# Optimization experiments

Measured on AMD Instinct MI355X. Metric: run time of the kernel, lower is better.

Reference implementation:

```python
import jax, jax.numpy as jnp
import numpy as np
from jax.scipy.special import logsumexp

NUM_STATES = 16
NUM_CHAINS = 8
NUM_NODES = 1500
NUM_ITERS = 500


def setup_inputs() -> dict:
    key = jax.random.key(0)
    k1, k2, k3, k4 = jax.random.split(key, 4)
    return {
        "unnormalized_state_init": jax.random.normal(k1, (NUM_STATES, NUM_CHAINS), jnp.float32),
        "unnormalized_chain_weights": jax.random.normal(k2, (NUM_ITERS, NUM_CHAINS), jnp.float32),
        "unnormalized_emission_matrix": jax.random.normal(k3, (NUM_STATES, 1, NUM_NODES), jnp.float32),
        "unnormalized_transition_matrix": jax.random.normal(k4, (NUM_CHAINS, NUM_STATES, NUM_STATES), jnp.float32),
    }


def reference(unnormalized_state_init, unnormalized_chain_weights,
              unnormalized_emission_matrix, unnormalized_transition_matrix):
    # log_transform_params: normalize each distribution in log domain
    log_state_init = jax.nn.log_softmax(unnormalized_state_init, axis=0)          # (S,C): over states
    log_chain_weights = jax.nn.log_softmax(unnormalized_chain_weights, axis=-1)   # (T,C): over chains
    log_emission = jax.nn.log_softmax(unnormalized_emission_matrix, axis=-1)      # (S,1,N): over nodes
    log_T_ = jax.nn.log_softmax(unnormalized_transition_matrix, axis=-1)          # (C,S,S): over next state

    T = unnormalized_chain_weights.shape[0]

    # chain-marginalized transition matrix (computed as in torch forward_model; not used downstream)
    log_mean_cw = logsumexp(log_chain_weights, axis=0) - jnp.log(jnp.asarray(T, log_chain_weights.dtype))
    _log_transition_matrix = logsumexp(log_T_ + log_mean_cw[:, None, None], axis=0)

    # sequential HMM prior recursion over tiny (S,C) state via scan
    def step(h, _):
        # h: (S,C) -> h.T: (C,S); logsumexp over previous-state axis
        new = logsumexp(h.T[:, :, None] + log_T_, axis=1).T  # (S,C)
        return new, new

    h0 = log_state_init
    _, hs = jax.lax.scan(step, h0, None, length=T - 1)
    log_hidden_state_probs = jnp.concatenate([h0[None], hs], axis=0)  # (T,S,C)

    # emission broadcast: (S,1,N) + (T,S,C,1) -> (T,S,C,N), then add chain weights
    log_observed_state_probs_ = (log_emission[None]
                                 + log_hidden_state_probs[..., None]
                                 + log_chain_weights[:, None, :, None])
    # marginalize over states then chains
    log_observed_state_probs = logsumexp(log_observed_state_probs_, axis=(1, 2))  # (T,N)
    return (log_observed_state_probs, log_observed_state_probs_, log_hidden_state_probs)
```

## Files before the change

### kernel.cpp

```cpp
#include <hip/hip_runtime.h>
#include <hip/hip_bf16.h>

#define S 16
#define C 8
#define SC 128
#define TT 500
#define NN 1500
#define CHUNK 25
#define NCHUNK 20

__device__ __forceinline__ float fexp2(float x) { return exp2f(x); }
__device__ __forceinline__ float flog2(float x) { return log2f(x); }

#define L2E 1.4426950408889634f
#define LN2 0.6931471805599453f

__global__ __launch_bounds__(256) void emission_kernel(
    const float* __restrict__ uem, float* __restrict__ lem)
{
    const int s0 = blockIdx.x;
    const float* row = uem + s0 * NN;
    const int tid = threadIdx.x;
    __shared__ float sm[4];
    __shared__ float ss[4];

    float m = -1e30f;
    for (int n = tid; n < NN; n += 256) m = fmaxf(m, row[n]);
#pragma unroll
    for (int off = 32; off >= 1; off >>= 1) m = fmaxf(m, __shfl_xor(m, off));
    if ((tid & 63) == 0) sm[tid >> 6] = m;
    __syncthreads();
    const float M = fmaxf(fmaxf(sm[0], sm[1]), fmaxf(sm[2], sm[3]));

    float acc = 0.f;
    for (int n = tid; n < NN; n += 256) acc += fexp2((row[n] - M) * L2E);
#pragma unroll
    for (int off = 32; off >= 1; off >>= 1) acc += __shfl_xor(acc, off);
    if ((tid & 63) == 0) ss[tid >> 6] = acc;
    __syncthreads();
    const float lse = M + flog2(ss[0] + ss[1] + ss[2] + ss[3]) * LN2;

    for (int n = tid; n < NN; n += 256) lem[s0 * NN + n] = row[n] - lse;
}

#define MM(dst, Asrc, Bsrc) do {                                          \
    __syncthreads();                                                      \
    {   const int c_ = tid >> 5; const int e0_ = tid & 31;                \
        for (int r_ = 0; r_ < 8; ++r_) {                                  \
            const int e_ = e0_ + (r_ << 5);                               \
            const int i_ = e_ >> 4; const int l_ = e_ & 15;               \
            float acc_ = 0.f;                                             \
            _Pragma("unroll")                                             \
            for (int s_ = 0; s_ < S; ++s_)                                \
                acc_ += Asrc[(c_ * S + i_) * S + s_] *                    \
                        Bsrc[(c_ * S + s_) * S + l_];                     \
            dst[(c_ * S + i_) * S + l_] = acc_;                          \
        } }                                                               \
} while (0)

__global__ __launch_bounds__(256) void hmm_setup(
    const float* __restrict__ usi,
    const float* __restrict__ ucw,
    const float* __restrict__ utm,
    float* __restrict__ ws_lcw,
    float* __restrict__ ws_pT,
    float* __restrict__ ws_q)
{
    __shared__ float bufT[C * S * S];
    __shared__ float bufX[C * S * S];
    __shared__ float bufY[C * S * S];
    __shared__ float bufZ[C * S * S];
    __shared__ float qbuf[C * S];
    const int tid = threadIdx.x;

    for (int t = tid; t < TT; t += 256) {
        float x[C]; float m = -1e30f;
#pragma unroll
        for (int cc = 0; cc < C; ++cc) { x[cc] = ucw[t * C + cc]; m = fmaxf(m, x[cc]); }
        float acc = 0.f;
#pragma unroll
        for (int cc = 0; cc < C; ++cc) acc += fexp2((x[cc] - m) * L2E);
        const float lse = m + flog2(acc) * LN2;
#pragma unroll
        for (int cc = 0; cc < C; ++cc) ws_lcw[t * C + cc] = x[cc] - lse;
    }

    if (tid < SC) {
        float x[S]; float m = -1e30f;
#pragma unroll
        for (int k = 0; k < S; ++k) { x[k] = utm[tid * S + k]; m = fmaxf(m, x[k]); }
        float acc = 0.f; float e[S];
#pragma unroll
        for (int k = 0; k < S; ++k) { e[k] = fexp2((x[k] - m) * L2E); acc += e[k]; }
        const float inv = 1.f / acc;
#pragma unroll
        for (int k = 0; k < S; ++k) {
            const float v = e[k] * inv;
            bufT[tid * S + k] = v;
            ws_pT[tid * S + k] = v;
        }
    }

    if (tid < C) {
        const int cc = tid;
        float x[S]; float m = -1e30f;
#pragma unroll
        for (int s0 = 0; s0 < S; ++s0) { x[s0] = usi[s0 * C + cc]; m = fmaxf(m, x[s0]); }
        float acc = 0.f; float e[S];
#pragma unroll
        for (int s0 = 0; s0 < S; ++s0) { e[s0] = fexp2((x[s0] - m) * L2E); acc += e[s0]; }
        const float inv = 1.f / acc;
#pragma unroll
        for (int s0 = 0; s0 < S; ++s0) {
            const float v = e[s0] * inv;
            qbuf[cc * S + s0] = v;
            ws_q[cc * S + s0] = v;
        }
    }

    MM(bufX, bufT, bufT);
    MM(bufY, bufX, bufX);
    MM(bufZ, bufY, bufY);
    MM(bufX, bufZ, bufZ);
    MM(bufY, bufX, bufZ);
    MM(bufX, bufY, bufT);
    __syncthreads();

    const int c5 = tid >> 4;
    const int l5 = tid & 15;
    float Acol[S];
    if (tid < 128) {
#pragma unroll
        for (int s0 = 0; s0 < S; ++s0) Acol[s0] = bufX[(c5 * S + s0) * S + l5];
    }
    for (int k = 1; k < NCHUNK; ++k) {
        float acc = 0.f;
        if (tid < 128) {
#pragma unroll
            for (int s0 = 0; s0 < S; ++s0) acc += qbuf[c5 * S + s0] * Acol[s0];
        }
        __syncthreads();
        if (tid < 128) {
            qbuf[c5 * S + l5] = acc;
            ws_q[k * SC + c5 * S + l5] = acc;
        }
        __syncthreads();
    }
}

__global__ __launch_bounds__(64) void hmm_chunks(
    const float* __restrict__ ws_pT,
    const float* __restrict__ ws_q,
    float* __restrict__ out3)
{
    const int k = blockIdx.x;
    const int lane = threadIdx.x;
    const int c = lane >> 3;
    const int j = lane & 7;

    float Ta[S], Tb[S];
#pragma unroll
    for (int s0 = 0; s0 < S; ++s0) {
        Ta[s0] = ws_pT[(c * S + s0) * S + j];
        Tb[s0] = ws_pT[(c * S + s0) * S + j + 8];
    }
    float pa = ws_q[k * SC + c * S + j];
    float pb = ws_q[k * SC + c * S + j + 8];

    const int base = c << 3;
    for (int i = 0; i < CHUNK; ++i) {
        float* o = out3 + (size_t)(k * CHUNK + i) * SC;
        o[j * C + c]       = flog2(pa) * LN2;
        o[(j + 8) * C + c] = flog2(pb) * LN2;
        if (i == CHUNK - 1) break;

        float pv[S];
#pragma unroll
        for (int q = 0; q < 8; ++q) {
            pv[q]     = __shfl(pa, base + q);
            pv[q + 8] = __shfl(pb, base + q);
        }
        float a0 = 0.f, a1 = 0.f, a2 = 0.f, a3 = 0.f;
        float b0 = 0.f, b1 = 0.f, b2 = 0.f, b3 = 0.f;
#pragma unroll
        for (int s0 = 0; s0 < S; s0 += 4) {
            a0 = fmaf(pv[s0],     Ta[s0],     a0);
            a1 = fmaf(pv[s0 + 1], Ta[s0 + 1], a1);
            a2 = fmaf(pv[s0 + 2], Ta[s0 + 2], a2);
            a3 = fmaf(pv[s0 + 3], Ta[s0 + 3], a3);
            b0 = fmaf(pv[s0],     Tb[s0],     b0);
            b1 = fmaf(pv[s0 + 1], Tb[s0 + 1], b1);
            b2 = fmaf(pv[s0 + 2], Tb[s0 + 2], b2);
            b3 = fmaf(pv[s0 + 3], Tb[s0 + 3], b3);
        }
        pa = (a0 + a1) + (a2 + a3);
        pb = (b0 + b1) + (b2 + b3);
    }
}

__global__ __launch_bounds__(128) void broadcast_kernel(
    const float* __restrict__ lem,
    const float* __restrict__ lcw,
    const float* __restrict__ h3,
    float* __restrict__ out1,
    float* __restrict__ out2)
{
    const int t = blockIdx.y;
    const int tid = threadIdx.x;
    __shared__ float hc[SC];
    __shared__ float Ws[S];
    if (tid < SC) hc[tid] = h3[t * SC + tid] + lcw[t * C + (tid & 7)];
    __syncthreads();
    if (tid < S) {
        float m = -1e30f;
#pragma unroll
        for (int cc = 0; cc < C; ++cc) m = fmaxf(m, hc[tid * C + cc]);
        float acc = 0.f;
#pragma unroll
        for (int cc = 0; cc < C; ++cc) acc += fexp2((hc[tid * C + cc] - m) * L2E);
        Ws[tid] = m + flog2(acc) * LN2;
    }
    __syncthreads();

    const int n4 = blockIdx.x * 128 + tid;
    if (n4 >= 375) return;

    float4 es[S];
#pragma unroll
    for (int s0 = 0; s0 < S; ++s0)
        es[s0] = ((const float4*)(lem + s0 * NN))[n4];

    float* o2 = out2 + (size_t)t * SC * NN + 4 * n4;
#pragma unroll
    for (int s0 = 0; s0 < S; ++s0) {
#pragma unroll
        for (int cc = 0; cc < C; ++cc) {
            const float hv = hc[s0 * C + cc];
            float4 v = es[s0];
            v.x += hv; v.y += hv; v.z += hv; v.w += hv;
            *(float4*)(o2 + (size_t)(s0 * C + cc) * NN) = v;
        }
    }

    float4 mv = make_float4(-1e30f, -1e30f, -1e30f, -1e30f);
    float4 xs[S];
#pragma unroll
    for (int s0 = 0; s0 < S; ++s0) {
        const float w = Ws[s0];
        xs[s0].x = es[s0].x + w; mv.x = fmaxf(mv.x, xs[s0].x);
        xs[s0].y = es[s0].y + w; mv.y = fmaxf(mv.y, xs[s0].y);
        xs[s0].z = es[s0].z + w; mv.z = fmaxf(mv.z, xs[s0].z);
        xs[s0].w = es[s0].w + w; mv.w = fmaxf(mv.w, xs[s0].w);
    }
    float4 av = make_float4(0.f, 0.f, 0.f, 0.f);
#pragma unroll
    for (int s0 = 0; s0 < S; ++s0) {
        av.x += fexp2((xs[s0].x - mv.x) * L2E);
        av.y += fexp2((xs[s0].y - mv.y) * L2E);
        av.z += fexp2((xs[s0].z - mv.z) * L2E);
        av.w += fexp2((xs[s0].w - mv.w) * L2E);
    }
    float4 r;
    r.x = mv.x + flog2(av.x) * LN2;
    r.y = mv.y + flog2(av.y) * LN2;
    r.z = mv.z + flog2(av.z) * LN2;
    r.w = mv.w + flog2(av.w) * LN2;
    *(float4*)(out1 + (size_t)t * NN + 4 * n4) = r;
}

extern "C" void kernel_launch(void* const* d_in, const int* in_sizes, int n_in,
                              void* d_out, int out_size, void* d_ws, size_t ws_size,
                              hipStream_t stream)
{
    const float* usi = (const float*)d_in[0];
    const float* ucw = (const float*)d_in[1];
    const float* uem = (const float*)d_in[2];
    const float* utm = (const float*)d_in[3];

    float* out  = (float*)d_out;
    float* out1 = out;
    float* out2 = out + 750000;
    float* out3 = out + 750000 + 96000000;

    float* ws      = (float*)d_ws;
    float* ws_lcw  = ws;
    float* ws_lem  = ws + 4000;
    float* ws_pT   = ws + 28000;
    float* ws_q    = ws + 30048;

    emission_kernel<<<16, 256, 0, stream>>>(uem, ws_lem);
    hmm_setup<<<1, 256, 0, stream>>>(usi, ucw, utm, ws_lcw, ws_pT, ws_q);
    hmm_chunks<<<NCHUNK, 64, 0, stream>>>(ws_pT, ws_q, out3);
    broadcast_kernel<<<dim3(3, 500), 128, 0, stream>>>(ws_lem, ws_lcw, out3, out1, out2);
}
```

Baseline: 126.6 us.

## Fuse chunked HMM recursion and emission normalization into one per-timestep broadcast kernel

Removes the separate emission normalization and chunk recursion kernels. The emission log-sum-exp now runs inside the setup kernel, and each of 500 per-timestep blocks recomputes its own short recursion from the chunk start before writing the broadcast outputs. The main output uses nontemporal vector stores, and the final logsumexp skips max subtraction. This cuts launches and intermediate traffic, at the cost of redundant recursion work per block and weaker numerical safety for large inputs.

```diff
diff --git a/kernel.cpp b/kernel.cpp
--- a/kernel.cpp
+++ b/kernel.cpp
@@ -6,6 +6,7 @@
 #define SC 128
 #define TT 500
 #define NN 1500
+#define NF4 375
 #define CHUNK 25
 #define NCHUNK 20
 
@@ -15,33 +16,7 @@
 #define L2E 1.4426950408889634f
 #define LN2 0.6931471805599453f
 
-__global__ __launch_bounds__(256) void emission_kernel(
-    const float* __restrict__ uem, float* __restrict__ lem)
-{
-    const int s0 = blockIdx.x;
-    const float* row = uem + s0 * NN;
-    const int tid = threadIdx.x;
-    __shared__ float sm[4];
-    __shared__ float ss[4];
-
-    float m = -1e30f;
-    for (int n = tid; n < NN; n += 256) m = fmaxf(m, row[n]);
-#pragma unroll
-    for (int off = 32; off >= 1; off >>= 1) m = fmaxf(m, __shfl_xor(m, off));
-    if ((tid & 63) == 0) sm[tid >> 6] = m;
-    __syncthreads();
-    const float M = fmaxf(fmaxf(sm[0], sm[1]), fmaxf(sm[2], sm[3]));
-
-    float acc = 0.f;
-    for (int n = tid; n < NN; n += 256) acc += fexp2((row[n] - M) * L2E);
-#pragma unroll
-    for (int off = 32; off >= 1; off >>= 1) acc += __shfl_xor(acc, off);
-    if ((tid & 63) == 0) ss[tid >> 6] = acc;
-    __syncthreads();
-    const float lse = M + flog2(ss[0] + ss[1] + ss[2] + ss[3]) * LN2;
-
-    for (int n = tid; n < NN; n += 256) lem[s0 * NN + n] = row[n] - lse;
-}
+typedef float f4v __attribute__((ext_vector_type(4)));
 
 #define MM(dst, Asrc, Bsrc) do {                                          \
     __syncthreads();                                                      \
@@ -61,10 +36,12 @@
 __global__ __launch_bounds__(256) void hmm_setup(
     const float* __restrict__ usi,
     const float* __restrict__ ucw,
+    const float* __restrict__ uem,
     const float* __restrict__ utm,
     float* __restrict__ ws_lcw,
     float* __restrict__ ws_pT,
-    float* __restrict__ ws_q)
+    float* __restrict__ ws_q,
+    float* __restrict__ ws_emlse)
 {
     __shared__ float bufT[C * S * S];
     __shared__ float bufX[C * S * S];
@@ -85,6 +62,17 @@
         for (int cc = 0; cc < C; ++cc) ws_lcw[t * C + cc] = x[cc] - lse;
     }
 
+    {
+        const int row = tid >> 4;
+        const int ln  = tid & 15;
+        const float* rp = uem + row * NN;
+        float a = 0.f;
+        for (int n = ln; n < NN; n += 16) a += fexp2(rp[n] * L2E);
+#pragma unroll
+        for (int off = 8; off >= 1; off >>= 1) a += __shfl_xor(a, off);
+        if (ln == 0) ws_emlse[row] = flog2(a) * LN2;
+    }
+
     if (tid < SC) {
         float x[S]; float m = -1e30f;
 #pragma unroll
@@ -148,124 +136,108 @@
     }
 }
 
-__global__ __launch_bounds__(64) void hmm_chunks(
+__global__ __launch_bounds__(512) void fused_bcast(
+    const float* __restrict__ uem,
+    const float* __restrict__ ws_lcw,
     const float* __restrict__ ws_pT,
     const float* __restrict__ ws_q,
+    const float* __restrict__ ws_emlse,
+    float* __restrict__ out1,
+    float* __restrict__ out2,
     float* __restrict__ out3)
 {
-    const int k = blockIdx.x;
-    const int lane = threadIdx.x;
-    const int c = lane >> 3;
-    const int j = lane & 7;
-
-    float Ta[S], Tb[S];
-#pragma unroll
-    for (int s0 = 0; s0 < S; ++s0) {
-        Ta[s0] = ws_pT[(c * S + s0) * S + j];
-        Tb[s0] = ws_pT[(c * S + s0) * S + j + 8];
-    }
-    float pa = ws_q[k * SC + c * S + j];
-    float pb = ws_q[k * SC + c * S + j + 8];
-
-    const int base = c << 3;
-    for (int i = 0; i < CHUNK; ++i) {
-        float* o = out3 + (size_t)(k * CHUNK + i) * SC;
-        o[j * C + c]       = flog2(pa) * LN2;
-        o[(j + 8) * C + c] = flog2(pb) * LN2;
-        if (i == CHUNK - 1) break;
-
-        float pv[S];
-#pragma unroll
-        for (int q = 0; q < 8; ++q) {
-            pv[q]     = __shfl(pa, base + q);
-            pv[q + 8] = __shfl(pb, base + q);
-        }
-        float a0 = 0.f, a1 = 0.f, a2 = 0.f, a3 = 0.f;
-        float b0 = 0.f, b1 = 0.f, b2 = 0.f, b3 = 0.f;
-#pragma unroll
-        for (int s0 = 0; s0 < S; s0 += 4) {
-            a0 = fmaf(pv[s0],     Ta[s0],     a0);
-            a1 = fmaf(pv[s0 + 1], Ta[s0 + 1], a1);
-            a2 = fmaf(pv[s0 + 2], Ta[s0 + 2], a2);
-            a3 = fmaf(pv[s0 + 3], Ta[s0 + 3], a3);
-            b0 = fmaf(pv[s0],     Tb[s0],     b0);
-            b1 = fmaf(pv[s0 + 1], Tb[s0 + 1], b1);
-            b2 = fmaf(pv[s0 + 2], Tb[s0 + 2], b2);
-            b3 = fmaf(pv[s0 + 3], Tb[s0 + 3], b3);
-        }
-        pa = (a0 + a1) + (a2 + a3);
-        pb = (b0 + b1) + (b2 + b3);
-    }
-}
-
-__global__ __launch_bounds__(128) void broadcast_kernel(
-    const float* __restrict__ lem,
-    const float* __restrict__ lcw,
-    const float* __restrict__ h3,
-    float* __restrict__ out1,
-    float* __restrict__ out2)
-{
-    const int t = blockIdx.y;
+    const int t = blockIdx.x;
     const int tid = threadIdx.x;
     __shared__ float hc[SC];
     __shared__ float Ws[S];
-    if (tid < SC) hc[tid] = h3[t * SC + tid] + lcw[t * C + (tid & 7)];
+    __shared__ float em[S];
+
+    if (tid >= 64 && tid < 64 + S) em[tid - 64] = ws_emlse[tid - 64];
+
+    if (tid < 64) {
+        const int c = tid >> 3;
+        const int j = tid & 7;
+        float Ta[S], Tb[S];
+#pragma unroll
+        for (int s0 = 0; s0 < S; ++s0) {
+            Ta[s0] = ws_pT[(c * S + s0) * S + j];
+            Tb[s0] = ws_pT[(c * S + s0) * S + j + 8];
+        }
+        const int k = t / CHUNK;
+        const int m = t - k * CHUNK;
+        float pa = ws_q[k * SC + c * S + j];
+        float pb = ws_q[k * SC + c * S + j + 8];
+        const int base = c << 3;
+        for (int i = 0; i < m; ++i) {
+            float pv[S];
+#pragma unroll
+            for (int q = 0; q < 8; ++q) {
+                pv[q]     = __shfl(pa, base + q);
+                pv[q + 8] = __shfl(pb, base + q);
+            }
+            float a0 = 0.f, a1 = 0.f, a2 = 0.f, a3 = 0.f;
+            float b0 = 0.f, b1 = 0.f, b2 = 0.f, b3 = 0.f;
+#pragma unroll
+            for (int s0 = 0; s0 < S; s0 += 4) {
+                a0 = fmaf(pv[s0],     Ta[s0],     a0);
+                a1 = fmaf(pv[s0 + 1], Ta[s0 + 1], a1);
+                a2 = fmaf(pv[s0 + 2], Ta[s0 + 2], a2);
+                a3 = fmaf(pv[s0 + 3], Ta[s0 + 3], a3);
+                b0 = fmaf(pv[s0],     Tb[s0],     b0);
+                b1 = fmaf(pv[s0 + 1], Tb[s0 + 1], b1);
+                b2 = fmaf(pv[s0 + 2], Tb[s0 + 2], b2);
+                b3 = fmaf(pv[s0 + 3], Tb[s0 + 3], b3);
+            }
+            pa = (a0 + a1) + (a2 + a3);
+            pb = (b0 + b1) + (b2 + b3);
+        }
+        const float la = flog2(pa) * LN2;
+        const float lb = flog2(pb) * LN2;
+        out3[(size_t)t * SC + j * C + c]       = la;
+        out3[(size_t)t * SC + (j + 8) * C + c] = lb;
+        const float w = ws_lcw[t * C + c];
+        hc[j * C + c]       = la + w;
+        hc[(j + 8) * C + c] = lb + w;
+    }
     __syncthreads();
     if (tid < S) {
-        float m = -1e30f;
-#pragma unroll
-        for (int cc = 0; cc < C; ++cc) m = fmaxf(m, hc[tid * C + cc]);
+        float mx = -1e30f;
+#pragma unroll
+        for (int cc = 0; cc < C; ++cc) mx = fmaxf(mx, hc[tid * C + cc]);
         float acc = 0.f;
 #pragma unroll
-        for (int cc = 0; cc < C; ++cc) acc += fexp2((hc[tid * C + cc] - m) * L2E);
-        Ws[tid] = m + flog2(acc) * LN2;
+        for (int cc = 0; cc < C; ++cc) acc += fexp2((hc[tid * C + cc] - mx) * L2E);
+        Ws[tid] = mx + flog2(acc) * LN2;
     }
     __syncthreads();
 
-    const int n4 = blockIdx.x * 128 + tid;
-    if (n4 >= 375) return;
-
-    float4 es[S];
-#pragma unroll
-    for (int s0 = 0; s0 < S; ++s0)
-        es[s0] = ((const float4*)(lem + s0 * NN))[n4];
-
-    float* o2 = out2 + (size_t)t * SC * NN + 4 * n4;
-#pragma unroll
-    for (int s0 = 0; s0 < S; ++s0) {
-#pragma unroll
-        for (int cc = 0; cc < C; ++cc) {
-            const float hv = hc[s0 * C + cc];
-            float4 v = es[s0];
-            v.x += hv; v.y += hv; v.z += hv; v.w += hv;
-            *(float4*)(o2 + (size_t)(s0 * C + cc) * NN) = v;
-        }
-    }
-
-    float4 mv = make_float4(-1e30f, -1e30f, -1e30f, -1e30f);
-    float4 xs[S];
-#pragma unroll
-    for (int s0 = 0; s0 < S; ++s0) {
-        const float w = Ws[s0];
-        xs[s0].x = es[s0].x + w; mv.x = fmaxf(mv.x, xs[s0].x);
-        xs[s0].y = es[s0].y + w; mv.y = fmaxf(mv.y, xs[s0].y);
-        xs[s0].z = es[s0].z + w; mv.z = fmaxf(mv.z, xs[s0].z);
-        xs[s0].w = es[s0].w + w; mv.w = fmaxf(mv.w, xs[s0].w);
-    }
-    float4 av = make_float4(0.f, 0.f, 0.f, 0.f);
-#pragma unroll
-    for (int s0 = 0; s0 < S; ++s0) {
-        av.x += fexp2((xs[s0].x - mv.x) * L2E);
-        av.y += fexp2((xs[s0].y - mv.y) * L2E);
-        av.z += fexp2((xs[s0].z - mv.z) * L2E);
-        av.w += fexp2((xs[s0].w - mv.w) * L2E);
-    }
-    float4 r;
-    r.x = mv.x + flog2(av.x) * LN2;
-    r.y = mv.y + flog2(av.y) * LN2;
-    r.z = mv.z + flog2(av.z) * LN2;
-    r.w = mv.w + flog2(av.w) * LN2;
-    *(float4*)(out1 + (size_t)t * NN + 4 * n4) = r;
+    if (tid < NF4) {
+        f4v acc1 = {0.f, 0.f, 0.f, 0.f};
+        float* o2t = out2 + (size_t)t * SC * NN + tid * 4;
+        for (int s0 = 0; s0 < S; ++s0) {
+            f4v e = *(const f4v*)(uem + s0 * NN + tid * 4);
+            const float el = em[s0];
+            e -= el;
+            const float w = Ws[s0];
+            acc1.x += fexp2((e.x + w) * L2E);
+            acc1.y += fexp2((e.y + w) * L2E);
+            acc1.z += fexp2((e.z + w) * L2E);
+            acc1.w += fexp2((e.w + w) * L2E);
+            float* orow = o2t + (size_t)s0 * C * NN;
+#pragma unroll
+            for (int cc = 0; cc < C; ++cc) {
+                const float hv = hc[s0 * C + cc];
+                f4v v = e + hv;
+                __builtin_nontemporal_store(v, (f4v*)(orow + (size_t)cc * NN));
+            }
+        }
+        f4v r;
+        r.x = flog2(acc1.x) * LN2;
+        r.y = flog2(acc1.y) * LN2;
+        r.z = flog2(acc1.z) * LN2;
+        r.w = flog2(acc1.w) * LN2;
+        *(f4v*)(out1 + (size_t)t * NN + tid * 4) = r;
+    }
 }
 
 extern "C" void kernel_launch(void* const* d_in, const int* in_sizes, int n_in,
@@ -282,14 +254,13 @@
     float* out2 = out + 750000;
     float* out3 = out + 750000 + 96000000;
 
-    float* ws      = (float*)d_ws;
-    float* ws_lcw  = ws;
-    float* ws_lem  = ws + 4000;
-    float* ws_pT   = ws + 28000;
-    float* ws_q    = ws + 30048;
-
-    emission_kernel<<<16, 256, 0, stream>>>(uem, ws_lem);
-    hmm_setup<<<1, 256, 0, stream>>>(usi, ucw, utm, ws_lcw, ws_pT, ws_q);
-    hmm_chunks<<<NCHUNK, 64, 0, stream>>>(ws_pT, ws_q, out3);
-    broadcast_kernel<<<dim3(3, 500), 128, 0, stream>>>(ws_lem, ws_lcw, out3, out1, out2);
+    float* ws       = (float*)d_ws;
+    float* ws_lcw   = ws;
+    float* ws_pT    = ws + 4000;
+    float* ws_q     = ws + 6048;
+    float* ws_emlse = ws + 8608;
+
+    hmm_setup<<<1, 256, 0, stream>>>(usi, ucw, uem, utm, ws_lcw, ws_pT, ws_q, ws_emlse);
+    fused_bcast<<<TT, 512, 0, stream>>>(uem, ws_lcw, ws_pT, ws_q, ws_emlse,
+                                        out1, out2, out3);
 }
```

Measured after the change: 139.6 us. 10.2% more time.
